# Kernel tuning notes

Measured on AMD Instinct MI355X. Metric: run time of the kernel, lower is better.

The kernel has to match this reference:

```python
import jax, jax.numpy as jnp
import numpy as np

B, C, H, W = 65536, 105, 3, 3  # C=105 forced by reshape(-1,15,7); H=W=3 forced by conv(k=2)+pool(2)->1x1


def setup_inputs() -> dict:
    key = jax.random.key(0)
    kx, kw, kb = jax.random.split(key, 3)
    x = jax.random.normal(kx, (B, C, H, W), dtype=jnp.float32)
    # Inject zero pixels (as produced by upstream zero-padding in SQUARE-Mamba)
    # so the nearest-neighbor fill path is exercised; the mask is read from x[0,0].
    x = x.at[:, :, 0, 0].set(0.0).at[:, :, 2, 2].set(0.0)
    # torch Conv2d default init: U(-1/sqrt(fan_in), +), depthwise fan_in = 1*2*2 = 4
    bound = 1.0 / np.sqrt(4.0)
    w = jax.random.uniform(kw, (C, 1, 2, 2), jnp.float32, -bound, bound)
    b = jax.random.uniform(kb, (C,), jnp.float32, -bound, bound)
    return {"x": x, "w": w, "b": b}


def nearest_padding(x):
    # Mask comes from sample 0, channel 0 only; fill applies to ALL batch/channels.
    Bn, Cn, Hn, Wn = x.shape
    P = Hn * Wn
    mflat = (x[0, 0] == 0).ravel()                                  # [P] True = zero pixel
    ii, jj = jnp.meshgrid(jnp.arange(Hn), jnp.arange(Wn), indexing="ij")
    coords = jnp.stack([ii.ravel(), jj.ravel()], axis=-1)           # [P,2] int32
    d = ((coords[:, None, :] - coords[None, :, :]) ** 2).sum(-1)    # [P,P] squared dist
    big = jnp.array(np.iinfo(np.int32).max, d.dtype)
    d = jnp.where(mflat[None, :], big, d)                           # exclude zero pixels as sources
    # argmin ties -> lowest flat (row-major) index, matching torch's argmin over
    # the row-major-ordered nonzero index list.
    nearest = jnp.argmin(d, axis=1)                                 # [P]
    xf = x.reshape(Bn, Cn, P)
    filled = jnp.where(mflat[None, None, :], xf[:, :, nearest], xf)
    return filled.reshape(Bn, Cn, Hn, Wn)


def reference(x, w, b):
    aug = nearest_padding(x)                                        # [B,C,3,3]
    y = jax.lax.conv_general_dilated(
        aug, w, window_strides=(1, 1), padding="VALID",
        dimension_numbers=("NCHW", "OIHW", "NCHW"),
        feature_group_count=C)                                      # depthwise -> [B,C,2,2]
    y = y + b[None, :, None, None]
    y = jnp.where(y > 0, y, 0.2 * y)                                # LeakyReLU(0.2)
    y = y.max(axis=(2, 3))                                          # MaxPool2d(2) -> [B,C]
    y = y + aug[:, :, 1, 1]
    return y.reshape(-1, 15, 7)                                     # [B,15,7]
```

## Files before the change

### kernel.cpp

```cpp
#include <hip/hip_runtime.h>


#define NC 105
#define GPB 512

__global__ __launch_bounds__(256) void se_kernel(const float* __restrict__ x,
                                                 const float* __restrict__ w,
                                                 const float* __restrict__ b,
                                                 float* __restrict__ out) {
    __shared__ float sx[GPB * 9];
    __shared__ unsigned int s_nearpk[2] __attribute__((aligned(8)));

    const int tid = threadIdx.x;
    const int gbase = blockIdx.x * GPB;
    const float4* x4 = (const float4*)(x + (long long)gbase * 9);
    float4* sx4 = (float4*)sx;

    sx4[tid]       = x4[tid];
    sx4[tid + 256] = x4[tid + 256];
    sx4[tid + 512] = x4[tid + 512];
    sx4[tid + 768] = x4[tid + 768];
    if (tid < 128) sx4[tid + 1024] = x4[tid + 1024];

    if (tid == 0) {
        float m0[9];
        #pragma unroll
        for (int p = 0; p < 9; ++p) m0[p] = x[p];
        bool mask[9];
        #pragma unroll
        for (int p = 0; p < 9; ++p) mask[p] = (m0[p] == 0.0f);
        unsigned int lo = 0, hi = 0;
        #pragma unroll
        for (int p = 0; p < 9; ++p) {
            int np = p;
            if (mask[p]) {
                int best = 0x7fffffff, bq = 0;
                const int pi = p / 3, pj = p % 3;
                for (int q = 0; q < 9; ++q) {
                    if (mask[q]) continue;
                    const int qi = q / 3, qj = q % 3;
                    const int d = (pi - qi) * (pi - qi) + (pj - qj) * (pj - qj);
                    if (d < best) { best = d; bq = q; }
                }
                np = bq;
            }
            if (p < 8) lo |= (unsigned)np << (4 * p); else hi = (unsigned)np;
        }
        s_nearpk[0] = lo;
        s_nearpk[1] = hi;
    }
    __syncthreads();

    const unsigned int lo = s_nearpk[0];
    const unsigned int hi = s_nearpk[1];
    int nr[9];
    #pragma unroll
    for (int p = 0; p < 8; ++p) nr[p] = (lo >> (4 * p)) & 15;
    nr[8] = hi & 15;

    const float4* w4 = (const float4*)w;

    #pragma unroll
    for (int half = 0; half < 2; ++half) {
        const int gl = tid + half * 256;
        const int gidx = gbase + gl;
        const int c = gidx % NC;

        const float* a = &sx[gl * 9];
        float v[9];
        #pragma unroll
        for (int p = 0; p < 9; ++p) v[p] = a[nr[p]];

        const float4 wc = w4[c];
        const float bias = b[c];

        float y00 = fmaf(v[0], wc.x, fmaf(v[1], wc.y, fmaf(v[3], wc.z, v[4] * wc.w))) + bias;
        float y01 = fmaf(v[1], wc.x, fmaf(v[2], wc.y, fmaf(v[4], wc.z, v[5] * wc.w))) + bias;
        float y10 = fmaf(v[3], wc.x, fmaf(v[4], wc.y, fmaf(v[6], wc.z, v[7] * wc.w))) + bias;
        float y11 = fmaf(v[4], wc.x, fmaf(v[5], wc.y, fmaf(v[7], wc.z, v[8] * wc.w))) + bias;

        y00 = (y00 > 0.0f) ? y00 : 0.2f * y00;
        y01 = (y01 > 0.0f) ? y01 : 0.2f * y01;
        y10 = (y10 > 0.0f) ? y10 : 0.2f * y10;
        y11 = (y11 > 0.0f) ? y11 : 0.2f * y11;

        const float m = fmaxf(fmaxf(y00, y01), fmaxf(y10, y11));
        out[gidx] = m + v[4];
    }
}

extern "C" void kernel_launch(void* const* d_in, const int* in_sizes, int n_in,
                              void* d_out, int out_size, void* d_ws, size_t ws_size,
                              hipStream_t stream) {
    const float* x = (const float*)d_in[0];
    const float* w = (const float*)d_in[1];
    const float* b = (const float*)d_in[2];
    float* out = (float*)d_out;

    const int n_groups = in_sizes[0] / 9;
    const int grid = n_groups / GPB;

    se_kernel<<<grid, 256, 0, stream>>>(x, w, b, out);
}
```

Measured before the change: 336.8 us.

## Precompute nearest-fill map in separate kernel and make smem staging wave-local

After: 339.6 us. No clear change (+0.8%).

```diff
diff --git a/kernel.cpp b/kernel.cpp
--- a/kernel.cpp
+++ b/kernel.cpp
@@ -4,67 +4,65 @@
 #define NC 105
 #define GPB 512
 
+__global__ void se_map_kernel(const float* __restrict__ x,
+                              unsigned long long* __restrict__ mapout) {
+    bool mask[9];
+    #pragma unroll
+    for (int p = 0; p < 9; ++p) mask[p] = (x[p] == 0.0f);
+    unsigned long long pk = 0;
+    #pragma unroll
+    for (int p = 0; p < 9; ++p) {
+        int np = p;
+        if (mask[p]) {
+            int best = 0x7fffffff, bq = 0;
+            const int pi = p / 3, pj = p % 3;
+            for (int q = 0; q < 9; ++q) {
+                if (mask[q]) continue;
+                const int qi = q / 3, qj = q % 3;
+                const int d = (pi - qi) * (pi - qi) + (pj - qj) * (pj - qj);
+                if (d < best) { best = d; bq = q; }
+            }
+            np = bq;
+        }
+        pk |= (unsigned long long)np << (4 * p);
+    }
+    *mapout = pk;
+}
+
 __global__ __launch_bounds__(256) void se_kernel(const float* __restrict__ x,
                                                  const float* __restrict__ w,
                                                  const float* __restrict__ b,
+                                                 const unsigned long long* __restrict__ mapp,
                                                  float* __restrict__ out) {
     __shared__ float sx[GPB * 9];
-    __shared__ unsigned int s_nearpk[2] __attribute__((aligned(8)));
 
-    const int tid = threadIdx.x;
+    const int tid  = threadIdx.x;
+    const int lane = tid & 63;
+    const int wv   = tid >> 6;
     const int gbase = blockIdx.x * GPB;
+
     const float4* x4 = (const float4*)(x + (long long)gbase * 9);
     float4* sx4 = (float4*)sx;
 
-    sx4[tid]       = x4[tid];
-    sx4[tid + 256] = x4[tid + 256];
-    sx4[tid + 512] = x4[tid + 512];
-    sx4[tid + 768] = x4[tid + 768];
-    if (tid < 128) sx4[tid + 1024] = x4[tid + 1024];
+    const int fb = wv * 288;
+    sx4[fb + lane]       = x4[fb + lane];
+    sx4[fb + lane + 64]  = x4[fb + lane + 64];
+    sx4[fb + lane + 128] = x4[fb + lane + 128];
+    sx4[fb + lane + 192] = x4[fb + lane + 192];
+    if (lane < 32) sx4[fb + lane + 256] = x4[fb + lane + 256];
 
-    if (tid == 0) {
-        float m0[9];
-        #pragma unroll
-        for (int p = 0; p < 9; ++p) m0[p] = x[p];
-        bool mask[9];
-        #pragma unroll
-        for (int p = 0; p < 9; ++p) mask[p] = (m0[p] == 0.0f);
-        unsigned int lo = 0, hi = 0;
-        #pragma unroll
-        for (int p = 0; p < 9; ++p) {
-            int np = p;
-            if (mask[p]) {
-                int best = 0x7fffffff, bq = 0;
-                const int pi = p / 3, pj = p % 3;
-                for (int q = 0; q < 9; ++q) {
-                    if (mask[q]) continue;
-                    const int qi = q / 3, qj = q % 3;
-                    const int d = (pi - qi) * (pi - qi) + (pj - qj) * (pj - qj);
-                    if (d < best) { best = d; bq = q; }
-                }
-                np = bq;
-            }
-            if (p < 8) lo |= (unsigned)np << (4 * p); else hi = (unsigned)np;
-        }
-        s_nearpk[0] = lo;
-        s_nearpk[1] = hi;
-    }
-    __syncthreads();
-
-    const unsigned int lo = s_nearpk[0];
-    const unsigned int hi = s_nearpk[1];
+    const unsigned long long pk = *mapp;
     int nr[9];
     #pragma unroll
-    for (int p = 0; p < 8; ++p) nr[p] = (lo >> (4 * p)) & 15;
-    nr[8] = hi & 15;
+    for (int p = 0; p < 9; ++p) nr[p] = (int)((pk >> (4 * p)) & 15);
 
     const float4* w4 = (const float4*)w;
 
     #pragma unroll
     for (int half = 0; half < 2; ++half) {
-        const int gl = tid + half * 256;
+        const int gl   = wv * 128 + half * 64 + lane;
         const int gidx = gbase + gl;
-        const int c = gidx % NC;
+        const int c    = gidx % NC;
 
         const float* a = &sx[gl * 9];
         float v[9];
@@ -96,9 +94,11 @@
     const float* w = (const float*)d_in[1];
     const float* b = (const float*)d_in[2];
     float* out = (float*)d_out;
+    unsigned long long* map = (unsigned long long*)d_ws;
 
     const int n_groups = in_sizes[0] / 9;
     const int grid = n_groups / GPB;
 
-    se_kernel<<<grid, 256, 0, stream>>>(x, w, b, out);
+    se_map_kernel<<<1, 1, 0, stream>>>(x, map);
+    se_kernel<<<grid, 256, 0, stream>>>(x, w, b, map, out);
 }
```
